# Optimization experiments

Measured on AMD Instinct MI355X. Metric: run time of the kernel, lower is better.

Reference implementation:

```python
import jax, jax.numpy as jnp
import numpy as np

# Compressed weight shape [O, I] represents a dense [m=2*O, k=2*I] matrix:
#  - 1:2 structured row sparsity: `indices` [O] gives the nonzero dense row ids
#  - 2:4 structured col sparsity: `metadata` [O, I] gives, for each compressed
#    element, its position (0..3) within its group of 4 dense columns
O, I = 4096, 2048          # compressed weight dims (out_features, in_features)
M_DIM, K_DIM = 2 * O, 2 * I  # dense GEMM dims m, k
N_TOK = 4096               # n = input.shape[0]
K_ACT = 2048               # number of active activation rows (multiple of 64)
PAD_MULT = 64


def setup_inputs() -> dict:
    key = jax.random.key(0)
    k1, k2, k3, k4, k5 = jax.random.split(key, 5)
    inp = jax.random.normal(k1, (N_TOK, K_ACT), dtype=jnp.float32)
    # unique, sorted active-feature indices into the dense k dimension
    idx = jnp.sort(jax.random.permutation(k2, K_DIM)[:K_ACT]).astype(jnp.int32)
    # compressed N:M weight values (original uses torch.rand -> uniform [0,1))
    weight = jax.random.uniform(k3, (O, I), dtype=jnp.float32)
    # 1:2 row sparsity: which O of the m dense rows are nonzero
    indices = jnp.sort(jax.random.permutation(k4, M_DIM)[:O]).astype(jnp.int32)
    # 2:4 metadata: per group of 4 dense columns, 2 distinct sorted positions
    G = I // 2
    scores = jax.random.uniform(k5, (O, G, 4))
    metadata = jnp.sort(jnp.argsort(scores, axis=-1)[..., :2], axis=-1)
    metadata = metadata.reshape(O, I).astype(jnp.int32)
    return {"input": inp, "idx": idx, "weight": weight,
            "indices": indices, "metadata": metadata}


def _padding_idx(idx, mult):
    # pad index list to a multiple of `mult` (static shapes)
    pad = (-idx.shape[0]) % mult
    return jnp.pad(idx, (0, pad)), pad


def reference(input, idx, weight, indices, metadata):
    O_, I_ = weight.shape
    m, k, n = 2 * O_, 2 * I_, input.shape[0]
    # ---- decompress N:M weight to dense [m, k] ----
    group_base = (jnp.arange(I_) // 2) * 4                 # [I]
    dense_cols = group_base[None, :] + metadata            # [O, I] in [0, k)
    W = jnp.zeros((m, k), weight.dtype).at[indices[:, None], dense_cols].set(weight)
    # ---- decompress sparse activation to dense B [k, n] ----
    idx_p, pad = _padding_idx(idx, PAD_MULT)
    vals = jnp.pad(input, ((0, 0), (0, pad)))              # [n, K_act+pad]
    B = jnp.zeros((k, n), input.dtype).at[idx_p].add(vals.T)
    # ---- sparse-sparse GEMM (dense-equivalent reference) ----
    return W @ B                                           # [m, n]
```

## Files before the change

### kernel.cpp

```cpp
#include <hip/hip_runtime.h>
#include <hip/hip_bf16.h>
#include <stdint.h>

#define O_DIM   4096
#define I_DIM   2048
#define M_DENSE 8192
#define K_DENSE 4096
#define N_TOK   4096
#define K_ACT   2048

typedef __bf16 bf16x8 __attribute__((ext_vector_type(8)));
typedef float  f32x4  __attribute__((ext_vector_type(4)));

__device__ __forceinline__ unsigned short f2bf(float f) {
    unsigned u = __builtin_bit_cast(unsigned, f);
    unsigned r = (u + 0x7FFFu + ((u >> 16) & 1u)) >> 16;
    return (unsigned short)r;
}

__device__ __forceinline__ void load16(const unsigned short* g, unsigned short* l) {
    __builtin_amdgcn_global_load_lds(
        (__attribute__((address_space(1))) void*)(g),
        (__attribute__((address_space(3))) void*)(l),
        16, 0, 0);
}

__global__ void build_inv(const int* __restrict__ idx, int* __restrict__ inv) {
    int c = blockIdx.x * blockDim.x + threadIdx.x;
    if (c >= K_DENSE) return;
    int lo = 0, hi = K_ACT;
    while (lo < hi) { int mid = (lo + hi) >> 1; if (idx[mid] < c) lo = mid + 1; else hi = mid; }
    inv[c] = (lo < K_ACT && idx[lo] == c) ? lo : -1;
}

__global__ void decompress_w(const float* __restrict__ weight,
                             const int* __restrict__ metadata,
                             const int* __restrict__ inv,
                             unsigned short* __restrict__ A2) {
    int gid = blockIdx.x * blockDim.x + threadIdx.x;
    int o = gid >> 10;
    int g = gid & 1023;
    size_t base = (size_t)o * I_DIM + 2 * g;
    int2   meta = *(const int2*)(metadata + base);
    float2 wv   = *(const float2*)(weight + base);
    int cbase = g * 4;
    size_t arow = (size_t)o * K_ACT;
#pragma unroll
    for (int c4 = 0; c4 < 4; ++c4) {
        int j = inv[cbase + c4];
        if (j >= 0) {
            float val = (meta.x == c4) ? wv.x : ((meta.y == c4) ? wv.y : 0.0f);
            A2[arow + j] = f2bf(val);
        }
    }
}

__global__ void cast_b(const float4* __restrict__ in, unsigned short* __restrict__ outb) {
    int i = blockIdx.x * blockDim.x + threadIdx.x;
    float4 v = in[i];
    ushort4 u;
    u.x = f2bf(v.x); u.y = f2bf(v.y); u.z = f2bf(v.z); u.w = f2bf(v.w);
    *(ushort4*)(outb + (size_t)i * 4) = u;
}

__global__ void gemm_scatter(const unsigned short* __restrict__ A,
                             const unsigned short* __restrict__ Bt,
                             const int* __restrict__ indices,
                             float* __restrict__ out) {
    constexpr int N = N_TOK, K = K_ACT;
    constexpr int TM = 128, TN = 128, BK = 32;
    __shared__ alignas(16) unsigned short sA[TM * BK];
    __shared__ alignas(16) unsigned short sB[TN * BK];

    const int t    = threadIdx.x;
    const int wave = t >> 6;
    const int lane = t & 63;
    const int m0 = blockIdx.y * TM;
    const int n0 = blockIdx.x * TN;

    const int fa0 = t, fa1 = t + 256;
    const unsigned short* gA0 = A  + (size_t)(m0 + (fa0 >> 2)) * K + (fa0 & 3) * 8;
    const unsigned short* gA1 = A  + (size_t)(m0 + (fa1 >> 2)) * K + (fa1 & 3) * 8;
    const unsigned short* gB0 = Bt + (size_t)(n0 + (fa0 >> 2)) * K + (fa0 & 3) * 8;
    const unsigned short* gB1 = Bt + (size_t)(n0 + (fa1 >> 2)) * K + (fa1 & 3) * 8;

    unsigned short* lA0 = sA + wave * 512;
    unsigned short* lA1 = sA + 2048 + wave * 512;
    unsigned short* lB0 = sB + wave * 512;
    unsigned short* lB1 = sB + 2048 + wave * 512;

    const int wm   = (wave >> 1) * 64;
    const int wn   = (wave & 1) * 64;
    const int quad = lane >> 4;
    const int lr   = lane & 15;
    const int kq   = quad * 8;

    f32x4 acc[4][4] = {};

    for (int kk = 0; kk < K; kk += BK) {
        __syncthreads();
        load16(gA0 + kk, lA0);
        load16(gA1 + kk, lA1);
        load16(gB0 + kk, lB0);
        load16(gB1 + kk, lB1);
        __syncthreads();

        bf16x8 af[4], bf[4];
#pragma unroll
        for (int mi = 0; mi < 4; ++mi)
            af[mi] = *(const bf16x8*)(sA + (wm + mi * 16 + lr) * BK + kq);
#pragma unroll
        for (int ni = 0; ni < 4; ++ni)
            bf[ni] = *(const bf16x8*)(sB + (wn + ni * 16 + lr) * BK + kq);
#pragma unroll
        for (int mi = 0; mi < 4; ++mi)
#pragma unroll
            for (int ni = 0; ni < 4; ++ni)
                acc[mi][ni] = __builtin_amdgcn_mfma_f32_16x16x32_bf16(
                    af[mi], bf[ni], acc[mi][ni], 0, 0, 0);
    }

#pragma unroll
    for (int mi = 0; mi < 4; ++mi) {
#pragma unroll
        for (int r = 0; r < 4; ++r) {
            int gm = m0 + wm + mi * 16 + quad * 4 + r;
            int orow = indices[gm];
            float* op = out + (size_t)orow * N + n0 + wn + lr;
#pragma unroll
            for (int ni = 0; ni < 4; ++ni)
                op[ni * 16] = acc[mi][ni][r];
        }
    }
}

extern "C" void kernel_launch(void* const* d_in, const int* in_sizes, int n_in,
                              void* d_out, int out_size, void* d_ws, size_t ws_size,
                              hipStream_t stream) {
    const float* input    = (const float*)d_in[0];
    const int*   idx      = (const int*)d_in[1];
    const float* weight   = (const float*)d_in[2];
    const int*   indices  = (const int*)d_in[3];
    const int*   metadata = (const int*)d_in[4];
    float* out = (float*)d_out;

    unsigned short* A2  = (unsigned short*)d_ws;
    unsigned short* Bbt = (unsigned short*)((char*)d_ws + (size_t)(16 << 20));
    int*            inv = (int*)((char*)d_ws + (size_t)(32 << 20));

    hipMemsetAsync(out, 0, (size_t)out_size * sizeof(float), stream);

    build_inv<<<K_DENSE / 256, 256, 0, stream>>>(idx, inv);
    decompress_w<<<(O_DIM * (I_DIM / 2)) / 256, 256, 0, stream>>>(weight, metadata, inv, A2);
    cast_b<<<(N_TOK * K_ACT / 4) / 256, 256, 0, stream>>>((const float4*)input, Bbt);

    dim3 grid(N_TOK / 128, O_DIM / 128);
    gemm_scatter<<<grid, 256, 0, stream>>>(A2, Bbt, indices, out);
}
```

Measured before the change: 314.4 us.

## Zero only inactive output rows, gather-decompress weights, vectorize casts, swizzle LDS

The full output memset is replaced by a kernel that zeros only the rows not listed in `indices`, roughly halving the output write traffic. Weight decompression now gathers directly over the active columns using `idx`, writing packed 16-byte bf16 vectors, so the inverse-index kernel is no longer needed. The activation cast writes 16-byte packed stores. The GEMM also XOR-swizzles the LDS layout to reduce bank conflicts on fragment reads. The zero kernel does a binary search per block, and the gathered metadata and weight loads are less coalesced.

```diff
diff --git a/kernel.cpp b/kernel.cpp
--- a/kernel.cpp
+++ b/kernel.cpp
@@ -12,10 +12,9 @@
 typedef __bf16 bf16x8 __attribute__((ext_vector_type(8)));
 typedef float  f32x4  __attribute__((ext_vector_type(4)));
 
-__device__ __forceinline__ unsigned short f2bf(float f) {
+__device__ __forceinline__ unsigned f2bf(float f) {
     unsigned u = __builtin_bit_cast(unsigned, f);
-    unsigned r = (u + 0x7FFFu + ((u >> 16) & 1u)) >> 16;
-    return (unsigned short)r;
+    return (u + 0x7FFFu + ((u >> 16) & 1u)) >> 16;
 }
 
 __device__ __forceinline__ void load16(const unsigned short* g, unsigned short* l) {
@@ -25,42 +24,60 @@
         16, 0, 0);
 }
 
-__global__ void build_inv(const int* __restrict__ idx, int* __restrict__ inv) {
-    int c = blockIdx.x * blockDim.x + threadIdx.x;
-    if (c >= K_DENSE) return;
-    int lo = 0, hi = K_ACT;
-    while (lo < hi) { int mid = (lo + hi) >> 1; if (idx[mid] < c) lo = mid + 1; else hi = mid; }
-    inv[c] = (lo < K_ACT && idx[lo] == c) ? lo : -1;
+__global__ void zero_inactive(const int* __restrict__ indices, float4* __restrict__ out4) {
+    int row = blockIdx.y;
+    __shared__ int active;
+    if (threadIdx.x == 0) {
+        int lo = 0, hi = O_DIM;
+        while (lo < hi) { int mid = (lo + hi) >> 1; if (indices[mid] < row) lo = mid + 1; else hi = mid; }
+        active = (lo < O_DIM && indices[lo] == row) ? 1 : 0;
+    }
+    __syncthreads();
+    if (active) return;
+    int col4 = blockIdx.x * 256 + threadIdx.x;
+    out4[(size_t)row * (N_TOK / 4) + col4] = float4{0.f, 0.f, 0.f, 0.f};
 }
 
 __global__ void decompress_w(const float* __restrict__ weight,
                              const int* __restrict__ metadata,
-                             const int* __restrict__ inv,
-                             unsigned short* __restrict__ A2) {
+                             const int* __restrict__ idx,
+                             uint4* __restrict__ A2) {
     int gid = blockIdx.x * blockDim.x + threadIdx.x;
-    int o = gid >> 10;
-    int g = gid & 1023;
-    size_t base = (size_t)o * I_DIM + 2 * g;
-    int2   meta = *(const int2*)(metadata + base);
-    float2 wv   = *(const float2*)(weight + base);
-    int cbase = g * 4;
-    size_t arow = (size_t)o * K_ACT;
+    int o  = gid >> 8;
+    int j0 = (gid & 255) * 8;
+    const int*   mrow = metadata + (size_t)o * I_DIM;
+    const float* wrow = weight   + (size_t)o * I_DIM;
+    int4 c0 = *(const int4*)(idx + j0);
+    int4 c1 = *(const int4*)(idx + j0 + 4);
+    int cs[8] = {c0.x, c0.y, c0.z, c0.w, c1.x, c1.y, c1.z, c1.w};
+    unsigned r[8];
 #pragma unroll
-    for (int c4 = 0; c4 < 4; ++c4) {
-        int j = inv[cbase + c4];
-        if (j >= 0) {
-            float val = (meta.x == c4) ? wv.x : ((meta.y == c4) ? wv.y : 0.0f);
-            A2[arow + j] = f2bf(val);
-        }
+    for (int u = 0; u < 8; ++u) {
+        int c = cs[u];
+        int g2 = (c >> 2) * 2;
+        int pos = c & 3;
+        int2   mm = *(const int2*)(mrow + g2);
+        float2 ww = *(const float2*)(wrow + g2);
+        float v = (mm.x == pos) ? ww.x : ((mm.y == pos) ? ww.y : 0.0f);
+        r[u] = f2bf(v);
     }
+    uint4 packed;
+    packed.x = r[0] | (r[1] << 16);
+    packed.y = r[2] | (r[3] << 16);
+    packed.z = r[4] | (r[5] << 16);
+    packed.w = r[6] | (r[7] << 16);
+    A2[gid] = packed;
 }
 
-__global__ void cast_b(const float4* __restrict__ in, unsigned short* __restrict__ outb) {
-    int i = blockIdx.x * blockDim.x + threadIdx.x;
-    float4 v = in[i];
-    ushort4 u;
-    u.x = f2bf(v.x); u.y = f2bf(v.y); u.z = f2bf(v.z); u.w = f2bf(v.w);
-    *(ushort4*)(outb + (size_t)i * 4) = u;
+__global__ void cast_b(const float4* __restrict__ in, uint4* __restrict__ outb) {
+    int gid = blockIdx.x * blockDim.x + threadIdx.x;
+    float4 a = in[2 * gid], b = in[2 * gid + 1];
+    uint4 u;
+    u.x = f2bf(a.x) | (f2bf(a.y) << 16);
+    u.y = f2bf(a.z) | (f2bf(a.w) << 16);
+    u.z = f2bf(b.x) | (f2bf(b.y) << 16);
+    u.w = f2bf(b.z) | (f2bf(b.w) << 16);
+    outb[gid] = u;
 }
 
 __global__ void gemm_scatter(const unsigned short* __restrict__ A,
@@ -79,10 +96,12 @@
     const int n0 = blockIdx.x * TN;
 
     const int fa0 = t, fa1 = t + 256;
-    const unsigned short* gA0 = A  + (size_t)(m0 + (fa0 >> 2)) * K + (fa0 & 3) * 8;
-    const unsigned short* gA1 = A  + (size_t)(m0 + (fa1 >> 2)) * K + (fa1 & 3) * 8;
-    const unsigned short* gB0 = Bt + (size_t)(n0 + (fa0 >> 2)) * K + (fa0 & 3) * 8;
-    const unsigned short* gB1 = Bt + (size_t)(n0 + (fa1 >> 2)) * K + (fa1 & 3) * 8;
+    const int r0 = fa0 >> 2, s0 = (fa0 & 3) ^ (r0 & 3);
+    const int r1 = fa1 >> 2, s1 = (fa1 & 3) ^ (r1 & 3);
+    const unsigned short* gA0 = A  + (size_t)(m0 + r0) * K + s0 * 8;
+    const unsigned short* gA1 = A  + (size_t)(m0 + r1) * K + s1 * 8;
+    const unsigned short* gB0 = Bt + (size_t)(n0 + r0) * K + s0 * 8;
+    const unsigned short* gB1 = Bt + (size_t)(n0 + r1) * K + s1 * 8;
 
     unsigned short* lA0 = sA + wave * 512;
     unsigned short* lA1 = sA + 2048 + wave * 512;
@@ -93,7 +112,7 @@
     const int wn   = (wave & 1) * 64;
     const int quad = lane >> 4;
     const int lr   = lane & 15;
-    const int kq   = quad * 8;
+    const int kq   = (quad ^ (lr & 3)) * 8;
 
     f32x4 acc[4][4] = {};
 
@@ -146,13 +165,11 @@
 
     unsigned short* A2  = (unsigned short*)d_ws;
     unsigned short* Bbt = (unsigned short*)((char*)d_ws + (size_t)(16 << 20));
-    int*            inv = (int*)((char*)d_ws + (size_t)(32 << 20));
 
-    hipMemsetAsync(out, 0, (size_t)out_size * sizeof(float), stream);
-
-    build_inv<<<K_DENSE / 256, 256, 0, stream>>>(idx, inv);
-    decompress_w<<<(O_DIM * (I_DIM / 2)) / 256, 256, 0, stream>>>(weight, metadata, inv, A2);
-    cast_b<<<(N_TOK * K_ACT / 4) / 256, 256, 0, stream>>>((const float4*)input, Bbt);
+    zero_inactive<<<dim3(N_TOK / 1024, M_DENSE), 256, 0, stream>>>(indices, (float4*)out);
+    decompress_w<<<(O_DIM * K_ACT / 8) / 256, 256, 0, stream>>>(
+        weight, metadata, idx, (uint4*)A2);
+    cast_b<<<(N_TOK * K_ACT / 8) / 256, 256, 0, stream>>>((const float4*)input, (uint4*)Bbt);
 
     dim3 grid(N_TOK / 128, O_DIM / 128);
     gemm_scatter<<<grid, 256, 0, stream>>>(A2, Bbt, indices, out);
```

Result: slower. 349.2 us (+11.1%).
